# Kernel tuning notes

Hardware: AMD Instinct MI355X
Metric: run time of the kernel (lower is better)

Reference implementation:

```python
import jax, jax.numpy as jnp
import numpy as np

B, N, DIM = 32, 3136, 64
H, DH, AGENTS = 8, 8, 49
INNER = H * DH  # 64
SCALE = DH ** -0.5


def setup_inputs() -> dict:
    key = jax.random.key(0)
    ks = jax.random.split(key, 7)
    s = 0.05
    return {
        "x1": jax.random.normal(ks[0], (B, N, DIM), jnp.float32),
        "x2": jax.random.normal(ks[1], (B, N, INNER), jnp.float32),
        "Wq": jax.random.normal(ks[2], (INNER, DIM), jnp.float32) * s,   # to_q (out,in)
        "Wk": jax.random.normal(ks[3], (DIM, INNER), jnp.float32) * s,   # to_k
        "Wv": jax.random.normal(ks[4], (DIM, INNER), jnp.float32) * s,   # to_v
        "Wo": jax.random.normal(ks[5], (2 * DIM, 2 * DIM), jnp.float32) * s,  # to_out linear
        "bo": jax.random.normal(ks[6], (2 * DIM,), jnp.float32) * s,
    }


def _split_heads(t):
    # (b, n, h*d) -> (b, h, n, d)
    b, n, hd = t.shape
    return t.reshape(b, n, H, hd // H).transpose(0, 2, 1, 3)


def reference(x1, x2, Wq, Wk, Wv, Wo, bo):
    b, n, _ = x1.shape
    q = x1 @ Wq.T                      # (b, n, 64)
    k = x2 @ Wk.T                      # (b, n, dim=64)
    v = x2 @ Wv.T
    # AdaptiveAvgPool2d((49, dim)): n % 49 == 0 and channel 64->64 is identity,
    # so pooling is an exact block mean over the sequence axis.
    agent = q.reshape(b, AGENTS, n // AGENTS, q.shape[-1]).mean(axis=2)  # (b, 49, 64)

    agent_h = _split_heads(agent)      # (b, h, 49, d)
    q1 = _split_heads(q)               # (b, h, n, d)
    k_h = _split_heads(k)
    v_h = _split_heads(v)

    # stage 0: agent tokens attend over keys/values (dropout is identity at eval)
    dots0 = jnp.einsum('bhid,bhjd->bhij', agent_h, k_h) * SCALE   # (b,h,49,n)
    attn0 = jax.nn.softmax(dots0, axis=-1)
    out0 = jnp.einsum('bhij,bhjd->bhid', attn0, v_h)              # (b,h,49,d)

    # stage 1: queries attend over agent tokens
    dots1 = jnp.einsum('bhid,bhjd->bhij', q1, agent_h) * SCALE    # (b,h,n,49)
    attn1 = jax.nn.softmax(dots1, axis=-1)
    out1 = jnp.einsum('bhij,bhjd->bhid', attn1, out0)             # (b,h,n,d)

    out1 = out1.transpose(0, 2, 1, 3).reshape(b, n, -1)           # (b,n,64)
    out1 = jnp.concatenate([out1, x1], axis=-1)                   # (b,n,128)
    return out1 @ Wo.T + bo
```

## Files before the change

kernel.cpp:

```cpp
#include <hip/hip_runtime.h>
#include <hip/hip_bf16.h>

#define NB 32
#define NSEQ 3136
#define NDIM 64
#define NH 8
#define NAG 49
#define NPAIR 25

static constexpr float kScale = 0.35355339059327378f;
static constexpr float kLog2e = 1.4426950408889634f;

typedef unsigned short us;
typedef __attribute__((ext_vector_type(8))) __bf16 bf16x8;
typedef __attribute__((ext_vector_type(4))) __bf16 bf16x4;
typedef __attribute__((ext_vector_type(2))) _Float16 f16x2;
typedef __attribute__((ext_vector_type(4))) _Float16 f16x4;
typedef __attribute__((ext_vector_type(8))) _Float16 f16x8;
typedef __attribute__((ext_vector_type(4))) float f32x4;

__device__ __forceinline__ float fexp2(float x) {
#if __has_builtin(__builtin_amdgcn_exp2f)
  return __builtin_amdgcn_exp2f(x);
#else
  return exp2f(x);
#endif
}

__device__ __forceinline__ float frcp(float x) {
#if __has_builtin(__builtin_amdgcn_rcpf)
  return __builtin_amdgcn_rcpf(x);
#else
  return 1.f / x;
#endif
}

__device__ __forceinline__ unsigned pk2(float a, float b) {
#if __has_builtin(__builtin_amdgcn_cvt_pkrtz)
  return __builtin_bit_cast(unsigned, __builtin_amdgcn_cvt_pkrtz(a, b));
#else
  f16x2 v = {(_Float16)a, (_Float16)b};
  return __builtin_bit_cast(unsigned, v);
#endif
}

__device__ __forceinline__ bf16x8 ldw8(const float* W, int row, int c0, int ld) {
  const float4* p = (const float4*)(W + (size_t)row * ld + c0);
  float4 v0 = p[0], v1 = p[1];
  bf16x8 r;
  r[0]=(__bf16)v0.x; r[1]=(__bf16)v0.y; r[2]=(__bf16)v0.z; r[3]=(__bf16)v0.w;
  r[4]=(__bf16)v1.x; r[5]=(__bf16)v1.y; r[6]=(__bf16)v1.z; r[7]=(__bf16)v1.w;
  return r;
}

__global__ __launch_bounds__(256) void agent_x1_kernel(
    const float* __restrict__ x1, const float* __restrict__ Wq,
    us* __restrict__ x1bf, us* __restrict__ agf16) {
  __shared__ float red[4][64];
  __shared__ float marr[64];
  const int a = blockIdx.x, b = blockIdx.y, t = threadIdx.x;
  const int i64 = t & 63, cb = t >> 6;

  {
    const float4* s1 = (const float4*)(x1 + ((size_t)(b * NSEQ) + a * 64 + i64) * NDIM + cb * 16);
    float4 v0 = s1[0], v1 = s1[1], v2 = s1[2], v3 = s1[3];
    bf16x8 p0, p1;
    p0[0]=(__bf16)v0.x; p0[1]=(__bf16)v0.y; p0[2]=(__bf16)v0.z; p0[3]=(__bf16)v0.w;
    p0[4]=(__bf16)v1.x; p0[5]=(__bf16)v1.y; p0[6]=(__bf16)v1.z; p0[7]=(__bf16)v1.w;
    p1[0]=(__bf16)v2.x; p1[1]=(__bf16)v2.y; p1[2]=(__bf16)v2.z; p1[3]=(__bf16)v2.w;
    p1[4]=(__bf16)v3.x; p1[5]=(__bf16)v3.y; p1[6]=(__bf16)v3.z; p1[7]=(__bf16)v3.w;
    __bf16* dst = (__bf16*)x1bf;
    *(bf16x8*)(dst + ((((size_t)b * NAG + a) * 8 + cb * 2) * 64 + i64) * 8) = p0;
    *(bf16x8*)(dst + ((((size_t)b * NAG + a) * 8 + cb * 2 + 1) * 64 + i64) * 8) = p1;
  }
  {
    const float* xc = x1 + ((size_t)(b * NSEQ) + a * 64 + cb * 16) * NDIM + i64;
    float cs = 0.f;
#pragma unroll
    for (int i = 0; i < 16; ++i) cs += xc[i * NDIM];
    red[cb][i64] = cs;
  }
  __syncthreads();
  if (t < 64) marr[t] = red[0][t] + red[1][t] + red[2][t] + red[3][t];
  __syncthreads();
  if (t < 64) {
    const float4* wqr = (const float4*)(Wq + (size_t)t * NDIM);
    const float4* mm = (const float4*)marr;
    float s0 = 0.f;
#pragma unroll
    for (int i = 0; i < 16; ++i) {
      float4 wv4 = wqr[i], m4 = mm[i];
      s0 += wv4.x * m4.x + wv4.y * m4.y + wv4.z * m4.z + wv4.w * m4.w;
    }
    const float val = s0 * (kScale * kLog2e / 64.f);
    ((_Float16*)agf16)[(((size_t)b * NH + (t >> 3)) * NAG + a) * 8 + (t & 7)] =
        (_Float16)val;
  }
}

__global__ __launch_bounds__(256) void kv_stage0_kernel(
    const float* __restrict__ x2, const float* __restrict__ Wk,
    const float* __restrict__ Wv, const us* __restrict__ agf16,
    us* __restrict__ pvp) {
  __shared__ __align__(16) __bf16 xb[64][72];
  __shared__ __align__(16) _Float16 klds[4][64][24];
  __shared__ __align__(16) _Float16 vlds[4][18][72];
  __shared__ __align__(16) _Float16 plds[4][64][40];
  const int pair = blockIdx.x, b = blockIdx.y, t = threadIdx.x;
  const int i64 = t & 63, cb = t >> 6;
  const int w = cb, lr = (t >> 4) & 3, lc = t & 15;

  bf16x8 ak0 = ldw8(Wk, w * 16 + lc, lr * 8, NDIM);
  bf16x8 ak1 = ldw8(Wk, w * 16 + lc, 32 + lr * 8, NDIM);
  bf16x8 av0 = ldw8(Wv, w * 16 + lc, lr * 8, NDIM);
  bf16x8 av1 = ldw8(Wv, w * 16 + lc, 32 + lr * 8, NDIM);

  const size_t bh0 = (size_t)b * NH + 2 * w;
  f16x8 ba[2][4];
#pragma unroll
  for (int hh = 0; hh < 2; ++hh)
#pragma unroll
    for (int at = 0; at < 4; ++at) {
      f16x8 v = (f16x8)(_Float16)0.0f;
      if (lr == 0) {
        int row = at * 16 + lc; if (row > 48) row = 48;
        v = *(const f16x8*)(agf16 + (bh0 + hh) * (NAG * 8) + row * 8);
      }
      ba[hh][at] = v;
    }
  vlds[w][16][i64] = (_Float16)1.0f;

  f32x4 accPV[2][4];
#pragma unroll
  for (int hh = 0; hh < 2; ++hh)
#pragma unroll
    for (int i = 0; i < 4; ++i) accPV[hh][i] = (f32x4){0.f, 0.f, 0.f, 0.f};

  for (int cc = 0; cc < 2; ++cc) {
    const int a = pair * 2 + cc;
    if (a >= NAG) break;
    if (cc) __syncthreads();

    {
      const float4* s2 = (const float4*)(x2 + ((size_t)(b * NSEQ) + a * 64 + i64) * NDIM + cb * 16);
      float4 v0 = s2[0], v1 = s2[1], v2 = s2[2], v3 = s2[3];
      bf16x8 p0, p1;
      p0[0]=(__bf16)v0.x; p0[1]=(__bf16)v0.y; p0[2]=(__bf16)v0.z; p0[3]=(__bf16)v0.w;
      p0[4]=(__bf16)v1.x; p0[5]=(__bf16)v1.y; p0[6]=(__bf16)v1.z; p0[7]=(__bf16)v1.w;
      p1[0]=(__bf16)v2.x; p1[1]=(__bf16)v2.y; p1[2]=(__bf16)v2.z; p1[3]=(__bf16)v2.w;
      p1[4]=(__bf16)v3.x; p1[5]=(__bf16)v3.y; p1[6]=(__bf16)v3.z; p1[7]=(__bf16)v3.w;
      *(bf16x8*)&xb[i64][cb * 16] = p0; *(bf16x8*)&xb[i64][cb * 16 + 8] = p1;
    }
    __syncthreads();

    f32x4 acck[4], accv[4];
#pragma unroll
    for (int i = 0; i < 4; ++i) {
      acck[i] = (f32x4){0.f, 0.f, 0.f, 0.f};
      accv[i] = (f32x4){0.f, 0.f, 0.f, 0.f};
    }
#pragma unroll
    for (int nt = 0; nt < 4; ++nt) {
      bf16x8 x0 = *(const bf16x8*)&xb[nt * 16 + lc][lr * 8];
      bf16x8 x1f = *(const bf16x8*)&xb[nt * 16 + lc][32 + lr * 8];
      acck[nt] = __builtin_amdgcn_mfma_f32_16x16x32_bf16(ak0, x0, acck[nt], 0, 0, 0);
      acck[nt] = __builtin_amdgcn_mfma_f32_16x16x32_bf16(ak1, x1f, acck[nt], 0, 0, 0);
      accv[nt] = __builtin_amdgcn_mfma_f32_16x16x32_bf16(av0, x0, accv[nt], 0, 0, 0);
      accv[nt] = __builtin_amdgcn_mfma_f32_16x16x32_bf16(av1, x1f, accv[nt], 0, 0, 0);
    }
#pragma unroll
    for (int nt = 0; nt < 4; ++nt) {
      f16x4 pk4;
      pk4[0]=(_Float16)acck[nt][0]; pk4[1]=(_Float16)acck[nt][1];
      pk4[2]=(_Float16)acck[nt][2]; pk4[3]=(_Float16)acck[nt][3];
      *(f16x4*)&klds[w][nt * 16 + lc][lr * 4] = pk4;
#pragma unroll
      for (int j = 0; j < 4; ++j)
        vlds[w][lr * 4 + j][nt * 16 + lc] = (_Float16)accv[nt][j];
    }

#pragma unroll
    for (int hh = 0; hh < 2; ++hh) {
#pragma unroll
      for (int half = 0; half < 2; ++half) {
#pragma unroll
        for (int tb = 0; tb < 2; ++tb) {
          const int tokbase = half * 32 + tb * 16;
          f16x8 kf = *(const f16x8*)&klds[w][tokbase + lc][hh * 8];
#pragma unroll
          for (int at = 0; at < 4; ++at) {
            f32x4 sc = __builtin_amdgcn_mfma_f32_16x16x32_f16(
                kf, ba[hh][at], (f32x4){0.f, 0.f, 0.f, 0.f}, 0, 0, 0);
            unsigned u0 = pk2(fexp2(sc[0]), fexp2(sc[1]));
            unsigned u1 = pk2(fexp2(sc[2]), fexp2(sc[3]));
            unsigned long long q = ((unsigned long long)u1 << 32) | u0;
            *(unsigned long long*)&plds[w][at * 16 + lc][tb * 16 + lr * 4] = q;
          }
        }
        const int frow = (lc < 8) ? hh * 8 + lc : 16;
        f16x8 vf = *(const f16x8*)&vlds[w][frow][half * 32 + lr * 8];
#pragma unroll
        for (int at = 0; at < 4; ++at) {
          f16x8 pf = *(const f16x8*)&plds[w][at * 16 + lc][lr * 8];
          accPV[hh][at] =
              __builtin_amdgcn_mfma_f32_16x16x32_f16(pf, vf, accPV[hh][at], 0, 0, 0);
        }
      }
    }
  }

#pragma unroll
  for (int hh = 0; hh < 2; ++hh) {
    if (lc < 9) {
      _Float16* dst = (_Float16*)pvp + ((bh0 + hh) * NPAIR + pair) * 441;
#pragma unroll
      for (int at = 0; at < 4; ++at)
#pragma unroll
        for (int j = 0; j < 4; ++j) {
          const int ag = at * 16 + lr * 4 + j;
          if (ag < NAG) dst[ag * 9 + lc] = (_Float16)accPV[hh][at][j];
        }
    }
  }
}

__global__ __launch_bounds__(256) void aofin_kernel(
    const us* __restrict__ pvp, us* __restrict__ pvtF) {
  __shared__ float acc[441];
  const int h = blockIdx.x, b = blockIdx.y, t = threadIdx.x;
  const size_t bh = (size_t)b * NH + h;
  const _Float16* src = (const _Float16*)pvp + bh * (NPAIR * 441);
  for (int s = t; s < 441; s += 256) {
    float v = 0.f;
#pragma unroll 5
    for (int p = 0; p < NPAIR; ++p) v += (float)src[(size_t)p * 441 + s];
    acc[s] = v;
  }
  __syncthreads();
  if (t < 64) {
    us* col = pvtF + bh * 1024 + t;
    float inv = (t < NAG) ? frcp(acc[t * 9 + 8]) : 0.f;
#pragma unroll
    for (int f = 0; f < 8; ++f) {
      float val = (t < NAG) ? acc[t * 9 + f] * inv : 0.f;
      _Float16 hv = (_Float16)val;
      col[f * 64] = __builtin_bit_cast(us, hv);
    }
    col[8 * 64] = (t < NAG) ? (us)0x3C00 : (us)0;
#pragma unroll
    for (int f = 9; f < 16; ++f) col[f * 64] = 0;
  }
}

__global__ __launch_bounds__(512, 8) void stage1_out_kernel(
    const us* __restrict__ x1bf, const float* __restrict__ Wq,
    const us* __restrict__ agf16, const us* __restrict__ pvtF,
    const float* __restrict__ Wo, const float* __restrict__ bo,
    float* __restrict__ out) {
  __shared__ __align__(16) __bf16 xa[64][72];
  __shared__ __align__(16) us qcat[64][72];
  __shared__ __align__(16) _Float16 pW[8][16][72];
  const int tile = blockIdx.x, b = blockIdx.y;
  const int t = threadIdx.x, tokl = t & 63, h = t >> 6;
  const int w = h, lane = t & 63, lr = (lane >> 4) & 3, lc = lane & 15;
  const int mtile = w & 3, thalf = w >> 2;
  const size_t bh = (size_t)b * NH + w;

  bf16x8 wqf0 = ldw8(Wq, mtile * 16 + lc, lr * 8, NDIM);
  bf16x8 wqf1 = ldw8(Wq, mtile * 16 + lc, 32 + lr * 8, NDIM);

  f16x8 ba[4];
#pragma unroll
  for (int at = 0; at < 4; ++at) {
    f16x8 v = (f16x8)(_Float16)0.0f;
    if (lr == 0) {
      int row = at * 16 + lc; if (row > 48) row = 48;
      v = *(const f16x8*)(agf16 + bh * (NAG * 8) + row * 8);
    }
    ba[at] = v;
  }
  const us* pvb = pvtF + bh * 1024;
  f16x8 pvB0 = *(const f16x8*)(pvb + lc * 64 + lr * 8);
  f16x8 pvB1 = *(const f16x8*)(pvb + lc * 64 + 32 + lr * 8);

  {
    bf16x8 p = *(const bf16x8*)((const __bf16*)x1bf +
        ((((size_t)b * NAG + tile) * 8 + h) * 64 + tokl) * 8);
    *(bf16x8*)&xa[tokl][h * 8] = p;
  }
  __syncthreads();

  {
    f32x4 aq[2];
    aq[0] = (f32x4){0.f,0.f,0.f,0.f}; aq[1] = (f32x4){0.f,0.f,0.f,0.f};
#pragma unroll
    for (int nt = 0; nt < 2; ++nt) {
      bf16x8 bx0 = *(const bf16x8*)&xa[thalf * 32 + nt * 16 + lc][lr * 8];
      bf16x8 bx1 = *(const bf16x8*)&xa[thalf * 32 + nt * 16 + lc][32 + lr * 8];
      aq[nt] = __builtin_amdgcn_mfma_f32_16x16x32_bf16(wqf0, bx0, aq[nt], 0, 0, 0);
      aq[nt] = __builtin_amdgcn_mfma_f32_16x16x32_bf16(wqf1, bx1, aq[nt], 0, 0, 0);
    }
#pragma unroll
    for (int nt = 0; nt < 2; ++nt) {
      f16x4 pk;
      pk[0]=(_Float16)aq[nt][0]; pk[1]=(_Float16)aq[nt][1];
      pk[2]=(_Float16)aq[nt][2]; pk[3]=(_Float16)aq[nt][3];
      *(f16x4*)&qcat[thalf * 32 + nt * 16 + lc][mtile * 16 + lr * 4] = pk;
    }
  }
  __syncthreads();

  {
    _Float16* psw = &pW[w][0][0];
#pragma unroll 1
    for (int g = 0; g < 4; ++g) {
      f16x8 qf = *(const f16x8*)&qcat[g * 16 + lc][w * 8];
#pragma unroll
      for (int at = 0; at < 4; ++at) {
        f32x4 sc = __builtin_amdgcn_mfma_f32_16x16x32_f16(
            ba[at], qf, (f32x4){0.f, 0.f, 0.f, 0.f}, 0, 0, 0);
        unsigned u0 = pk2(fexp2(sc[0]), fexp2(sc[1]));
        unsigned u1 = pk2(fexp2(sc[2]), fexp2(sc[3]));
        unsigned long long qq = ((unsigned long long)u1 << 32) | u0;
        *(unsigned long long*)&psw[(size_t)lc * 72 + at * 16 + lr * 4] = qq;
      }
      f16x8 pA0 = *(const f16x8*)&psw[(size_t)lc * 72 + lr * 8];
      f16x8 pA1 = *(const f16x8*)&psw[(size_t)lc * 72 + 32 + lr * 8];
      f32x4 pv = __builtin_amdgcn_mfma_f32_16x16x32_f16(
          pvB0, pA0, (f32x4){0.f, 0.f, 0.f, 0.f}, 0, 0, 0);
      pv = __builtin_amdgcn_mfma_f32_16x16x32_f16(pvB1, pA1, pv, 0, 0, 0);
      float den = __shfl(pv[0], 32 + lc);
      float inv = frcp(den);
      if (lr < 2) {
        bf16x4 pc;
        pc[0] = (__bf16)(pv[0] * inv); pc[1] = (__bf16)(pv[1] * inv);
        pc[2] = (__bf16)(pv[2] * inv); pc[3] = (__bf16)(pv[3] * inv);
        *(bf16x4*)((__bf16*)&qcat[g * 16 + lc][0] + w * 8 + lr * 4) = pc;
      }
    }
  }

  bf16x8 wof0 = ldw8(Wo, w * 16 + lc, lr * 8, 128);
  bf16x8 wof1 = ldw8(Wo, w * 16 + lc, 32 + lr * 8, 128);
  bf16x8 wof2 = ldw8(Wo, w * 16 + lc, 64 + lr * 8, 128);
  bf16x8 wof3 = ldw8(Wo, w * 16 + lc, 96 + lr * 8, 128);
  f32x4 bv = *(const f32x4*)(bo + w * 16 + lr * 4);
  f32x4 acc[4];
#pragma unroll
  for (int i = 0; i < 4; ++i) acc[i] = (f32x4){0.f,0.f,0.f,0.f};
#pragma unroll
  for (int nt = 0; nt < 4; ++nt) {
    bf16x8 b0 = *(const bf16x8*)&xa[nt * 16 + lc][lr * 8];
    bf16x8 b1 = *(const bf16x8*)&xa[nt * 16 + lc][32 + lr * 8];
    acc[nt] = __builtin_amdgcn_mfma_f32_16x16x32_bf16(wof2, b0, acc[nt], 0, 0, 0);
    acc[nt] = __builtin_amdgcn_mfma_f32_16x16x32_bf16(wof3, b1, acc[nt], 0, 0, 0);
  }
  __syncthreads();

#pragma unroll
  for (int nt = 0; nt < 4; ++nt) {
    bf16x8 c0 = *(const bf16x8*)&qcat[nt * 16 + lc][lr * 8];
    bf16x8 c1 = *(const bf16x8*)&qcat[nt * 16 + lc][32 + lr * 8];
    acc[nt] = __builtin_amdgcn_mfma_f32_16x16x32_bf16(wof0, c0, acc[nt], 0, 0, 0);
    acc[nt] = __builtin_amdgcn_mfma_f32_16x16x32_bf16(wof1, c1, acc[nt], 0, 0, 0);
    f32x4 v = acc[nt] + bv;
    float* dst = out + ((size_t)b * NSEQ + tile * 64 + nt * 16 + lc) * 128 + w * 16 + lr * 4;
    *(f32x4*)dst = v;
  }
}

extern "C" void kernel_launch(void* const* d_in, const int* in_sizes, int n_in,
                              void* d_out, int out_size, void* d_ws, size_t ws_size,
                              hipStream_t stream) {
  (void)in_sizes; (void)n_in; (void)out_size; (void)ws_size;
  const float* x1 = (const float*)d_in[0];
  const float* x2 = (const float*)d_in[1];
  const float* Wq = (const float*)d_in[2];
  const float* Wk = (const float*)d_in[3];
  const float* Wv = (const float*)d_in[4];
  const float* Wo = (const float*)d_in[5];
  const float* bo = (const float*)d_in[6];
  float* out = (float*)d_out;

  us* x1bf = (us*)d_ws;
  us* agf16 = x1bf + (size_t)NB * NSEQ * 64;
  us* pvp = agf16 + (size_t)NB * NH * NAG * 8;
  us* pvtF = pvp + (size_t)NB * NH * NPAIR * 441;

  agent_x1_kernel<<<dim3(NAG, NB), 256, 0, stream>>>(x1, Wq, x1bf, agf16);
  kv_stage0_kernel<<<dim3(NPAIR, NB), 256, 0, stream>>>(x2, Wk, Wv, agf16, pvp);
  aofin_kernel<<<dim3(NH, NB), 256, 0, stream>>>(pvp, pvtF);
  stage1_out_kernel<<<dim3(NAG, NB), 512, 0, stream>>>(x1bf, Wq, agf16,
                                                       pvtF, Wo, bo, out);
}
```

Baseline: 75.40 us.

## Compute per-head Q in-wave with MFMA and shuffles, dropping qcat LDS round trip

Each wave now computes only its own head's 8 Q channels for each 16-token group, with duplicated Wq rows in the A operand. It rebuilds the f16x8 Q fragment through lane shuffles instead of writing Q to the shared qcat buffer and reading it back after a block barrier. This removes one __syncthreads and the LDS traffic for Q, and fully unrolls the group loop. In exchange the Q MFMA work is doubled because half of each 16-row tile is redundant, and register pressure may rise from the unrolling.

```diff
diff --git a/kernel.cpp b/kernel.cpp
--- a/kernel.cpp
+++ b/kernel.cpp
@@ -18,6 +18,7 @@
 typedef __attribute__((ext_vector_type(4))) _Float16 f16x4;
 typedef __attribute__((ext_vector_type(8))) _Float16 f16x8;
 typedef __attribute__((ext_vector_type(4))) float f32x4;
+typedef __attribute__((ext_vector_type(4))) unsigned uint4v;
 
 __device__ __forceinline__ float fexp2(float x) {
 #if __has_builtin(__builtin_amdgcn_exp2f)
@@ -263,11 +264,10 @@
   const int tile = blockIdx.x, b = blockIdx.y;
   const int t = threadIdx.x, tokl = t & 63, h = t >> 6;
   const int w = h, lane = t & 63, lr = (lane >> 4) & 3, lc = lane & 15;
-  const int mtile = w & 3, thalf = w >> 2;
   const size_t bh = (size_t)b * NH + w;
 
-  bf16x8 wqf0 = ldw8(Wq, mtile * 16 + lc, lr * 8, NDIM);
-  bf16x8 wqf1 = ldw8(Wq, mtile * 16 + lc, 32 + lr * 8, NDIM);
+  bf16x8 wqA0 = ldw8(Wq, w * 8 + (lc & 7), lr * 8, NDIM);
+  bf16x8 wqA1 = ldw8(Wq, w * 8 + (lc & 7), 32 + lr * 8, NDIM);
 
   f16x8 ba[4];
 #pragma unroll
@@ -291,30 +291,19 @@
   __syncthreads();
 
   {
-    f32x4 aq[2];
-    aq[0] = (f32x4){0.f,0.f,0.f,0.f}; aq[1] = (f32x4){0.f,0.f,0.f,0.f};
-#pragma unroll
-    for (int nt = 0; nt < 2; ++nt) {
-      bf16x8 bx0 = *(const bf16x8*)&xa[thalf * 32 + nt * 16 + lc][lr * 8];
-      bf16x8 bx1 = *(const bf16x8*)&xa[thalf * 32 + nt * 16 + lc][32 + lr * 8];
-      aq[nt] = __builtin_amdgcn_mfma_f32_16x16x32_bf16(wqf0, bx0, aq[nt], 0, 0, 0);
-      aq[nt] = __builtin_amdgcn_mfma_f32_16x16x32_bf16(wqf1, bx1, aq[nt], 0, 0, 0);
-    }
-#pragma unroll
-    for (int nt = 0; nt < 2; ++nt) {
-      f16x4 pk;
-      pk[0]=(_Float16)aq[nt][0]; pk[1]=(_Float16)aq[nt][1];
-      pk[2]=(_Float16)aq[nt][2]; pk[3]=(_Float16)aq[nt][3];
-      *(f16x4*)&qcat[thalf * 32 + nt * 16 + lc][mtile * 16 + lr * 4] = pk;
-    }
-  }
-  __syncthreads();
-
-  {
     _Float16* psw = &pW[w][0][0];
-#pragma unroll 1
+#pragma unroll
     for (int g = 0; g < 4; ++g) {
-      f16x8 qf = *(const f16x8*)&qcat[g * 16 + lc][w * 8];
+      bf16x8 bx0 = *(const bf16x8*)&xa[g * 16 + lc][lr * 8];
+      bf16x8 bx1 = *(const bf16x8*)&xa[g * 16 + lc][32 + lr * 8];
+      f32x4 aq = __builtin_amdgcn_mfma_f32_16x16x32_bf16(
+          wqA0, bx0, (f32x4){0.f,0.f,0.f,0.f}, 0, 0, 0);
+      aq = __builtin_amdgcn_mfma_f32_16x16x32_bf16(wqA1, bx1, aq, 0, 0, 0);
+      unsigned uq0 = pk2(aq[0], aq[1]);
+      unsigned uq1 = pk2(aq[2], aq[3]);
+      unsigned uq2 = __shfl(uq0, (lane + 16) & 63);
+      unsigned uq3 = __shfl(uq1, (lane + 16) & 63);
+      f16x8 qf = __builtin_bit_cast(f16x8, (uint4v){uq0, uq1, uq2, uq3});
 #pragma unroll
       for (int at = 0; at < 4; ++at) {
         f32x4 sc = __builtin_amdgcn_mfma_f32_16x16x32_f16(
```

Measured after the change: 79.59 us. 1.06x slower.
